# Kernel optimization log

Hardware: AMD Instinct MI355X
Metric: run time of the kernel (lower is better)

Reference implementation:

```python
import jax, jax.numpy as jnp
import numpy as np

H_DIM = 256
NUM_HEADS = 8
HEAD_DIM = H_DIM // NUM_HEADS
BN_EPS = 1e-5
SCALE = float(np.sqrt(HEAD_DIM))


def _lens():
    # 512 graphs, ragged vertex counts cycling 32/64/96/128 -> 40960 total rows
    return np.tile(np.array([32, 64, 96, 128], dtype=np.int64), 128)


def _pad(x, lens):
    # gather ragged rows of x [total, D] into padded [B, Lmax, D]; mask [B, Lmax]
    B = lens.shape[0]
    L = int(lens.max())
    off = np.zeros(B, np.int64)
    off[1:] = np.cumsum(lens)[:-1]
    pos = np.arange(L)
    idx = off[:, None] + np.minimum(pos[None, :], lens[:, None] - 1)
    mask = pos[None, :] < lens[:, None]
    return x[jnp.asarray(idx)], jnp.asarray(mask)


def _flat_idx(lens):
    # (graph_id, position) for every real row, to un-pad back to ragged layout
    b = np.repeat(np.arange(lens.shape[0]), lens)
    i = np.concatenate([np.arange(int(l)) for l in lens])
    return jnp.asarray(b), jnp.asarray(i)


def _forward(src_h, dst_h, src_lens, dst_lens,
             W1, b1, gamma1, beta1, W2, b2, gamma2, beta2):
    src_pad, src_mask = _pad(src_h, src_lens)   # [B, Ls, H]
    dst_pad, _ = _pad(dst_h, dst_lens)          # [B, Ld, H]
    B, Ls, _ = src_pad.shape
    Ld = dst_pad.shape[1]
    # NOTE: original torch code zips self.proj but never applies it, so
    # q = raw dst, k = v = raw src.  The .view(1, head_dim, heads, N) on the
    # channel-major tensor splits feature f as f = d*NUM_HEADS + h.
    q = dst_pad.reshape(B, Ld, HEAD_DIM, NUM_HEADS)
    k = src_pad.reshape(B, Ls, HEAD_DIM, NUM_HEADS)
    v = k
    scores = jnp.einsum('bndh,bmdh->bhnm', q, k) / SCALE
    scores = jnp.where(src_mask[:, None, None, :], scores, jnp.float32(-1e30))
    attn = jax.nn.softmax(scores, axis=-1)
    out = jnp.einsum('bhnm,bmdh->bndh', attn, v).reshape(B, Ld, H_DIM)
    bidx, iidx = _flat_idx(dst_lens)
    h_msg = out[bidx, iidx]                     # [total_dst, H] ragged again
    h = dst_h
    z = jnp.concatenate([h, h_msg], axis=-1)    # [N, 2H]
    y = z @ W1.T + b1
    y = gamma1 * (y - y.mean(0)) * jax.lax.rsqrt(y.var(0) + BN_EPS) + beta1
    y = jax.nn.relu(y)
    y = y @ W2.T + b2
    y = gamma2 * (y - y.mean(0)) * jax.lax.rsqrt(y.var(0) + BN_EPS) + beta2
    return h + y


def setup_inputs() -> dict:
    lens = _lens()
    N = int(lens.sum())
    ks = jax.random.split(jax.random.key(0), 4)
    return {
        'src_h': jax.random.normal(ks[0], (N, H_DIM), jnp.float32),
        'dst_h': jax.random.normal(ks[1], (N, H_DIM), jnp.float32),
        'src_num_verts': jnp.asarray(lens, jnp.int32),
        'dst_num_verts': jnp.asarray(lens, jnp.int32),
        'W1': jax.random.normal(ks[2], (H_DIM, 2 * H_DIM), jnp.float32) / np.float32(np.sqrt(2 * H_DIM)),
        'b1': jnp.zeros((H_DIM,), jnp.float32),
        'gamma1': jnp.ones((H_DIM,), jnp.float32),
        'beta1': jnp.zeros((H_DIM,), jnp.float32),
        'W2': jax.random.normal(ks[3], (H_DIM, H_DIM), jnp.float32) / np.float32(np.sqrt(H_DIM)),
        'b2': jnp.zeros((H_DIM,), jnp.float32),
        'gamma2': jnp.ones((H_DIM,), jnp.float32),
        'beta2': jnp.zeros((H_DIM,), jnp.float32),
    }


def reference(src_h, dst_h, src_num_verts, dst_num_verts,
              W1, b1, gamma1, beta1, W2, b2, gamma2, beta2):
    # segment lengths are static metadata (torch.split takes a Python list)
    src_lens = np.asarray(jax.device_get(src_num_verts), np.int64)
    dst_lens = np.asarray(jax.device_get(dst_num_verts), np.int64)
    return _forward(src_h, dst_h, src_lens, dst_lens,
                    W1, b1, gamma1, beta1, W2, b2, gamma2, beta2)
```

## Files before the change

kernel.cpp:

```cpp
#include <hip/hip_runtime.h>
#include <cstddef>

#define H 256
#define NHEADS 8
#define HD 32

typedef __attribute__((ext_vector_type(8))) short bf16x8;
typedef __attribute__((ext_vector_type(4))) float f32x4;

__device__ __forceinline__ float bf2f(unsigned short s) {
    unsigned u = ((unsigned)s) << 16; return __builtin_bit_cast(float, u);
}
__device__ __forceinline__ float bfe2f(short s) {
    unsigned u = ((unsigned)(unsigned short)s) << 16; return __builtin_bit_cast(float, u);
}
__device__ __forceinline__ unsigned short f2bf(float x) {
    unsigned u = __builtin_bit_cast(unsigned, x);
    u += 0x7fffu + ((u >> 16) & 1u);
    return (unsigned short)(u >> 16);
}
__device__ __forceinline__ void gl_lds16(const void* g, void* l) {
    __builtin_amdgcn_global_load_lds(
        (const __attribute__((address_space(1))) void*)g,
        (__attribute__((address_space(3))) void*)l, 16, 0, 0);
}

__global__ __launch_bounds__(512) void scan_zero_kernel(
    const int* __restrict__ slen, const int* __restrict__ dlen,
    int* __restrict__ soff, int* __restrict__ doff,
    float* __restrict__ stats, int B)
{
    __shared__ int ss[512], dd[512];
    const int t = threadIdx.x;
    const int sv = (t < B) ? slen[t] : 0;
    const int dv = (t < B) ? dlen[t] : 0;
    ss[t] = sv; dd[t] = dv;
    __syncthreads();
    for (int o = 1; o < 512; o <<= 1) {
        int a = (t >= o) ? ss[t - o] : 0;
        int b = (t >= o) ? dd[t - o] : 0;
        __syncthreads();
        ss[t] += a; dd[t] += b;
        __syncthreads();
    }
    if (t < B) { soff[t] = ss[t] - sv; doff[t] = dd[t] - dv; }
    stats[t] = 0.f;
    stats[t + 512] = 0.f;
}

__global__ __launch_bounds__(256) void prepass_kernel(
    const float* __restrict__ src, const float* __restrict__ dst,
    unsigned short* __restrict__ KT, unsigned short* __restrict__ VT2,
    unsigned short* __restrict__ QT, int N)
{
    __shared__ unsigned short pl[8 * 64 * 40];
    const int t = threadIdx.x;
    const int rb = blockIdx.x * 64;
    const int isrc = (blockIdx.y == 0);
    const float* __restrict__ in = isrc ? src : dst;
    unsigned short* __restrict__ T = isrc ? KT : QT;
    #pragma unroll
    for (int i = 0; i < 16; ++i) {
        const int idx = t + i * 256;
        const int row = idx >> 6, f4 = idx & 63;
        const float4 v = ((const float4*)in)[(size_t)(rb + row) * 64 + f4];
        const int f0 = f4 * 4, h0 = f0 & 7, d = f0 >> 3;
        pl[(h0 + 0) * 2560 + row * 40 + d] = f2bf(v.x);
        pl[(h0 + 1) * 2560 + row * 40 + d] = f2bf(v.y);
        pl[(h0 + 2) * 2560 + row * 40 + d] = f2bf(v.z);
        pl[(h0 + 3) * 2560 + row * 40 + d] = f2bf(v.w);
    }
    __syncthreads();
    #pragma unroll
    for (int i = 0; i < 8; ++i) {
        const int idx = t + i * 256;
        const int h = idx >> 8, rem = idx & 255, row = rem >> 2, c = rem & 3;
        const bf16x8 val = *(const bf16x8*)&pl[h * 2560 + row * 40 + c * 8];
        *(bf16x8*)&T[(size_t)(h * N + rb + row) * 32 + c * 8] = val;
    }
    if (isrc) {
        #pragma unroll
        for (int i = 0; i < 8; ++i) {
            const int idx = t + i * 256;
            const int h = idx >> 8, rem = idx & 255, d = rem >> 3, nc = rem & 7;
            unsigned short tmp[8];
            #pragma unroll
            for (int j = 0; j < 8; ++j) tmp[j] = pl[h * 2560 + (nc * 8 + j) * 40 + d];
            ushort4 lo, hi;
            lo.x = tmp[0]; lo.y = tmp[1]; lo.z = tmp[2]; lo.w = tmp[3];
            hi.x = tmp[4]; hi.y = tmp[5]; hi.z = tmp[6]; hi.w = tmp[7];
            *(ushort4*)&VT2[(size_t)(h * 32 + d) * N + rb + nc * 8] = lo;
            *(ushort4*)&VT2[(size_t)(h * 32 + d) * N + rb + nc * 8 + 4] = hi;
        }
    }
}

__global__ __launch_bounds__(256) void cvtW_kernel(
    const float* __restrict__ W1, const float* __restrict__ W2,
    unsigned short* __restrict__ W1p, unsigned short* __restrict__ W2bf)
{
    const int idx = blockIdx.x * 256 + threadIdx.x;
    if (idx < 131072) {
        const int kp = idx & 511, c = idx >> 9;
        const int half = kp >> 8, r = kp & 255, hh = r >> 5, d = r & 31;
        W1p[(size_t)c * 512 + kp] = f2bf(W1[(size_t)c * 512 + half * 256 + d * 8 + hh]);
    } else {
        const int i2 = idx - 131072;
        W2bf[i2] = f2bf(W2[i2]);
    }
}

template<int LS>
__device__ __forceinline__ void attn_body(
    const unsigned short* __restrict__ KT, const unsigned short* __restrict__ QT,
    const unsigned short* __restrict__ VT2, unsigned short* __restrict__ OT,
    unsigned short* __restrict__ Ps, int N, int so, int df, int Ld, int h, int lane)
{
    constexpr int MT = LS / 16, CH = LS / 32;
    const int lr = lane & 15, lq = lane >> 4;
    const float iscale = 0.17677669529663687f;

    bf16x8 kf[MT];
    #pragma unroll
    for (int mt = 0; mt < MT; ++mt)
        kf[mt] = *(const bf16x8*)&KT[(size_t)(h * N + so + mt * 16 + lr) * 32 + lq * 8];
    bf16x8 vf[CH][2];
    #pragma unroll
    for (int c = 0; c < CH; ++c)
        #pragma unroll
        for (int dt = 0; dt < 2; ++dt)
            vf[c][dt] = *(const bf16x8*)&VT2[(size_t)(h * 32 + dt * 16 + lr) * N + so + c * 32 + lq * 8];

    const int NT = Ld >> 4;
    for (int nt = 0; nt < NT; ++nt) {
        const bf16x8 qf = *(const bf16x8*)&QT[(size_t)(h * N + df + nt * 16 + lr) * 32 + lq * 8];
        f32x4 s[MT];
        #pragma unroll
        for (int mt = 0; mt < MT; ++mt) {
            f32x4 z = {0.f, 0.f, 0.f, 0.f};
            s[mt] = __builtin_amdgcn_mfma_f32_16x16x32_bf16(kf[mt], qf, z, 0, 0, 0);
        }
        float mx = -INFINITY;
        #pragma unroll
        for (int mt = 0; mt < MT; ++mt)
            mx = fmaxf(mx, fmaxf(fmaxf(s[mt][0], s[mt][1]), fmaxf(s[mt][2], s[mt][3])));
        mx = fmaxf(mx, __shfl_xor(mx, 16));
        mx = fmaxf(mx, __shfl_xor(mx, 32));
        const float mxi = mx * iscale;
        float sum = 0.f;
        #pragma unroll
        for (int mt = 0; mt < MT; ++mt) {
            #pragma unroll
            for (int r = 0; r < 4; ++r) {
                const float e = __expf(s[mt][r] * iscale - mxi);
                s[mt][r] = e; sum += e;
            }
        }
        sum += __shfl_xor(sum, 16);
        sum += __shfl_xor(sum, 32);
        const float rinv = 1.f / sum;
        #pragma unroll
        for (int mt = 0; mt < MT; ++mt) {
            uint2 p;
            p.x = ((unsigned)f2bf(s[mt][0])) | (((unsigned)f2bf(s[mt][1])) << 16);
            p.y = ((unsigned)f2bf(s[mt][2])) | (((unsigned)f2bf(s[mt][3])) << 16);
            *(uint2*)&Ps[lr * 136 + mt * 16 + lq * 4] = p;
        }
        __asm__ volatile("" ::: "memory");
        __builtin_amdgcn_wave_barrier();
        f32x4 o0 = {0.f, 0.f, 0.f, 0.f}, o1 = {0.f, 0.f, 0.f, 0.f};
        #pragma unroll
        for (int c = 0; c < CH; ++c) {
            const bf16x8 pa = *(const bf16x8*)&Ps[lr * 136 + c * 32 + lq * 8];
            o0 = __builtin_amdgcn_mfma_f32_16x16x32_bf16(pa, vf[c][0], o0, 0, 0, 0);
            o1 = __builtin_amdgcn_mfma_f32_16x16x32_bf16(pa, vf[c][1], o1, 0, 0, 0);
        }
        __asm__ volatile("" ::: "memory");
        __builtin_amdgcn_wave_barrier();
        #pragma unroll
        for (int r = 0; r < 4; ++r) {
            const float rv = __shfl(rinv, lq * 4 + r);
            const int row = df + nt * 16 + lq * 4 + r;
            OT[(size_t)(h * N + row) * 32 + lr]      = f2bf(o0[r] * rv);
            OT[(size_t)(h * N + row) * 32 + 16 + lr] = f2bf(o1[r] * rv);
        }
    }
}

__global__ __launch_bounds__(256) void attn_mfma(
    const unsigned short* __restrict__ KT, const unsigned short* __restrict__ QT,
    const unsigned short* __restrict__ VT2, unsigned short* __restrict__ OT,
    const int* __restrict__ soff, const int* __restrict__ doff,
    const int* __restrict__ slen, const int* __restrict__ dlen, int N)
{
    __shared__ unsigned short Ps[4][16 * 136];
    const int b = blockIdx.x >> 1, half = blockIdx.x & 1;
    const int w = threadIdx.x >> 6, lane = threadIdx.x & 63;
    const int h = half * 4 + w;
    const int Ls = slen[b], Ld = dlen[b], so = soff[b], df = doff[b];
    switch (Ls) {
        case 32:  attn_body<32> (KT, QT, VT2, OT, Ps[w], N, so, df, Ld, h, lane); break;
        case 64:  attn_body<64> (KT, QT, VT2, OT, Ps[w], N, so, df, Ld, h, lane); break;
        case 96:  attn_body<96> (KT, QT, VT2, OT, Ps[w], N, so, df, Ld, h, lane); break;
        default:  attn_body<128>(KT, QT, VT2, OT, Ps[w], N, so, df, Ld, h, lane); break;
    }
}

__global__ __launch_bounds__(256) void gemm1_mfma(
    const unsigned short* __restrict__ QT, const unsigned short* __restrict__ OT,
    const unsigned short* __restrict__ W, const float* __restrict__ bias,
    unsigned short* __restrict__ out, float* __restrict__ sum, float* __restrict__ sq,
    int N)
{
    __shared__ unsigned short Abuf[8 * 512];
    __shared__ unsigned short Bbuf[8 * 512];
    const int tid = threadIdx.x;
    const int w = tid >> 6, lane = tid & 63;
    const int rowBase = blockIdx.y * 128, colBase = blockIdx.x * 128;
    const int lr = lane & 15, lq = lane >> 4;
    const int wm = w >> 1, wn = w & 1;

    f32x4 acc[4][4];
    #pragma unroll
    for (int i = 0; i < 4; ++i)
        #pragma unroll
        for (int j = 0; j < 4; ++j) { f32x4 z = {0.f, 0.f, 0.f, 0.f}; acc[i][j] = z; }

    #pragma unroll
    for (int phase = 0; phase < 2; ++phase) {
        const unsigned short* __restrict__ Ap = phase ? OT : QT;
        const int wOff = phase * 256;
        for (int kb = 0; kb < 256; kb += 32) {
            const int hh = (kb >> 5) + (lq >> 2);
            const int dd = (lq & 3) * 8;
            #pragma unroll
            for (int s = 0; s < 2; ++s) {
                const int sub = 2 * w + s;
                const unsigned short* ga = Ap + (size_t)(hh * N + rowBase + sub * 16 + lr) * 32 + dd;
                gl_lds16(ga, &Abuf[sub * 512]);
                const unsigned short* gb = W + (size_t)(colBase + sub * 16 + lr) * 512 + wOff + kb + lq * 8;
                gl_lds16(gb, &Bbuf[sub * 512]);
            }
            __syncthreads();
            bf16x8 af[4], bf[4];
            #pragma unroll
            for (int i = 0; i < 4; ++i) af[i] = *(const bf16x8*)&Abuf[(wm * 4 + i) * 512 + lane * 8];
            #pragma unroll
            for (int j = 0; j < 4; ++j) bf[j] = *(const bf16x8*)&Bbuf[(wn * 4 + j) * 512 + lane * 8];
            #pragma unroll
            for (int i = 0; i < 4; ++i)
                #pragma unroll
                for (int j = 0; j < 4; ++j)
                    acc[i][j] = __builtin_amdgcn_mfma_f32_16x16x32_bf16(af[i], bf[j], acc[i][j], 0, 0, 0);
            __syncthreads();
        }
    }
    const int col0 = colBase + wn * 64;
    #pragma unroll
    for (int j = 0; j < 4; ++j) {
        const int col = col0 + j * 16 + lr;
        const float bv = bias[col];
        float cs = 0.f, cq = 0.f;
        #pragma unroll
        for (int i = 0; i < 4; ++i) {
            const int row0 = rowBase + wm * 64 + i * 16 + lq * 4;
            #pragma unroll
            for (int r = 0; r < 4; ++r) {
                const float v = acc[i][j][r] + bv;
                cs += v; cq += v * v;
                out[(size_t)(row0 + r) * 256 + col] = f2bf(v);
            }
        }
        cs += __shfl_xor(cs, 16); cs += __shfl_xor(cs, 32);
        cq += __shfl_xor(cq, 16); cq += __shfl_xor(cq, 32);
        if (lq == 0) { atomicAdd(&sum[col], cs); atomicAdd(&sq[col], cq); }
    }
}

__global__ __launch_bounds__(256) void gemm2_mfma(
    const unsigned short* __restrict__ A2,
    const unsigned short* __restrict__ W, const float* __restrict__ bias,
    unsigned short* __restrict__ out, float* __restrict__ sum, float* __restrict__ sq)
{
    __shared__ unsigned short Abuf[8 * 512];
    __shared__ unsigned short Bbuf[8 * 512];
    const int tid = threadIdx.x;
    const int w = tid >> 6, lane = tid & 63;
    const int rowBase = blockIdx.y * 128, colBase = blockIdx.x * 128;
    const int lr = lane & 15, lq = lane >> 4;
    const int wm = w >> 1, wn = w & 1;

    f32x4 acc[4][4];
    #pragma unroll
    for (int i = 0; i < 4; ++i)
        #pragma unroll
        for (int j = 0; j < 4; ++j) { f32x4 z = {0.f, 0.f, 0.f, 0.f}; acc[i][j] = z; }

    for (int kb = 0; kb < 256; kb += 32) {
        #pragma unroll
        for (int s = 0; s < 2; ++s) {
            const int sub = 2 * w + s;
            const unsigned short* ga = A2 + (size_t)(rowBase + sub * 16 + lr) * 256 + kb + lq * 8;
            gl_lds16(ga, &Abuf[sub * 512]);
            const unsigned short* gb = W + (size_t)(colBase + sub * 16 + lr) * 256 + kb + lq * 8;
            gl_lds16(gb, &Bbuf[sub * 512]);
        }
        __syncthreads();
        bf16x8 af[4], bf[4];
        #pragma unroll
        for (int i = 0; i < 4; ++i) af[i] = *(const bf16x8*)&Abuf[(wm * 4 + i) * 512 + lane * 8];
        #pragma unroll
        for (int j = 0; j < 4; ++j) bf[j] = *(const bf16x8*)&Bbuf[(wn * 4 + j) * 512 + lane * 8];
        #pragma unroll
        for (int i = 0; i < 4; ++i)
            #pragma unroll
            for (int j = 0; j < 4; ++j)
                acc[i][j] = __builtin_amdgcn_mfma_f32_16x16x32_bf16(af[i], bf[j], acc[i][j], 0, 0, 0);
        __syncthreads();
    }
    const int col0 = colBase + wn * 64;
    #pragma unroll
    for (int j = 0; j < 4; ++j) {
        const int col = col0 + j * 16 + lr;
        const float bv = bias[col];
        float cs = 0.f, cq = 0.f;
        #pragma unroll
        for (int i = 0; i < 4; ++i) {
            const int row0 = rowBase + wm * 64 + i * 16 + lq * 4;
            #pragma unroll
            for (int r = 0; r < 4; ++r) {
                const float v = acc[i][j][r] + bv;
                cs += v; cq += v * v;
                out[(size_t)(row0 + r) * 256 + col] = f2bf(v);
            }
        }
        cs += __shfl_xor(cs, 16); cs += __shfl_xor(cs, 32);
        cq += __shfl_xor(cq, 16); cq += __shfl_xor(cq, 32);
        if (lq == 0) { atomicAdd(&sum[col], cs); atomicAdd(&sq[col], cq); }
    }
}

__global__ __launch_bounds__(256) void bnrelu_kernel(
    const unsigned short* __restrict__ y1,
    const float* __restrict__ sum, const float* __restrict__ sq,
    const float* __restrict__ gamma, const float* __restrict__ beta,
    unsigned short* __restrict__ out, int n8, float invN)
{
    const int i = blockIdx.x * 256 + threadIdx.x;
    if (i >= n8) return;
    const int j0 = (i & 31) * 8;
    const bf16x8 yv = ((const bf16x8*)y1)[i];
    short res[8];
    #pragma unroll
    for (int j = 0; j < 8; ++j) {
        const float mean = sum[j0 + j] * invN;
        const float var  = sq[j0 + j] * invN - mean * mean;
        const float rstd = rsqrtf(var + 1e-5f);
        const float sc = gamma[j0 + j] * rstd;
        const float sh = beta[j0 + j] - mean * sc;
        res[j] = (short)f2bf(fmaxf(bfe2f(yv[j]) * sc + sh, 0.f));
    }
    bf16x8 o;
    #pragma unroll
    for (int j = 0; j < 8; ++j) o[j] = res[j];
    ((bf16x8*)out)[i] = o;
}

__global__ __launch_bounds__(256) void epilogue_kernel(
    const float* __restrict__ dst, const unsigned short* __restrict__ y2,
    const float* __restrict__ sum, const float* __restrict__ sq,
    const float* __restrict__ gamma, const float* __restrict__ beta,
    float* __restrict__ out, int n8, float invN)
{
    const int i = blockIdx.x * 256 + threadIdx.x;
    if (i >= n8) return;
    const int j0 = (i & 31) * 8;
    const bf16x8 yv = ((const bf16x8*)y2)[i];
    const float4 d0 = ((const float4*)dst)[2 * i];
    const float4 d1 = ((const float4*)dst)[2 * i + 1];
    float o[8];
    const float dv[8] = {d0.x, d0.y, d0.z, d0.w, d1.x, d1.y, d1.z, d1.w};
    #pragma unroll
    for (int j = 0; j < 8; ++j) {
        const float mean = sum[j0 + j] * invN;
        const float var  = sq[j0 + j] * invN - mean * mean;
        const float rstd = rsqrtf(var + 1e-5f);
        const float sc = gamma[j0 + j] * rstd;
        const float sh = beta[j0 + j] - mean * sc;
        o[j] = dv[j] + bfe2f(yv[j]) * sc + sh;
    }
    float4 o0, o1;
    o0.x = o[0]; o0.y = o[1]; o0.z = o[2]; o0.w = o[3];
    o1.x = o[4]; o1.y = o[5]; o1.z = o[6]; o1.w = o[7];
    ((float4*)out)[2 * i]     = o0;
    ((float4*)out)[2 * i + 1] = o1;
}

extern "C" void kernel_launch(void* const* d_in, const int* in_sizes, int n_in,
                              void* d_out, int out_size, void* d_ws, size_t ws_size,
                              hipStream_t stream)
{
    const float* src_h  = (const float*)d_in[0];
    const float* dst_h  = (const float*)d_in[1];
    const int*   slen   = (const int*)d_in[2];
    const int*   dlen   = (const int*)d_in[3];
    const float* W1     = (const float*)d_in[4];
    const float* b1     = (const float*)d_in[5];
    const float* gamma1 = (const float*)d_in[6];
    const float* beta1  = (const float*)d_in[7];
    const float* W2     = (const float*)d_in[8];
    const float* b2     = (const float*)d_in[9];
    const float* gamma2 = (const float*)d_in[10];
    const float* beta2  = (const float*)d_in[11];
    float* out = (float*)d_out;

    const int N = in_sizes[1] / H;
    const int B = in_sizes[2];

    char* base = (char*)d_ws;
    int*   soff   = (int*)(base + 0);
    int*   doff   = (int*)(base + 2048);
    float* stats  = (float*)(base + 4096);
    unsigned short* W1p  = (unsigned short*)(base + 16384);
    unsigned short* W2bf = (unsigned short*)(base + 16384 + 262144);
    const size_t S = (size_t)N * H * sizeof(unsigned short);
    char* big = base + (1 << 20);
    unsigned short* KT  = (unsigned short*)(big);
    unsigned short* VT2 = (unsigned short*)(big + S);
    unsigned short* QT  = (unsigned short*)(big + 2 * S);
    unsigned short* OT  = (unsigned short*)(big + 3 * S);
    unsigned short* y1bf = KT;
    unsigned short* a2   = VT2;
    unsigned short* y2bf = QT;

    const float invN = 1.0f / (float)N;

    scan_zero_kernel<<<1, 512, 0, stream>>>(slen, dlen, soff, doff, stats, B);

    prepass_kernel<<<dim3(N / 64, 2), 256, 0, stream>>>(src_h, dst_h, KT, VT2, QT, N);
    cvtW_kernel<<<768, 256, 0, stream>>>(W1, W2, W1p, W2bf);

    attn_mfma<<<B * 2, 256, 0, stream>>>(KT, QT, VT2, OT, soff, doff, slen, dlen, N);

    dim3 ggrid(H / 128, N / 128);
    gemm1_mfma<<<ggrid, 256, 0, stream>>>(QT, OT, W1p, b1, y1bf, stats + 0, stats + 256, N);

    const int n8 = N * H / 8;
    bnrelu_kernel<<<(n8 + 255) / 256, 256, 0, stream>>>(
        y1bf, stats + 0, stats + 256, gamma1, beta1, a2, n8, invN);

    gemm2_mfma<<<ggrid, 256, 0, stream>>>(a2, W2bf, b2, y2bf, stats + 512, stats + 768);

    epilogue_kernel<<<(n8 + 255) / 256, 256, 0, stream>>>(
        dst_h, y2bf, stats + 512, stats + 768, gamma2, beta2, out, n8, invN);
}
```

Measured before the change: 283.6 us.

## Fuse BN1+ReLU into GEMM2 and load MFMA operands directly from global

Drops the standalone BN/ReLU pass by applying the first batch-norm scale/shift and ReLU to Y1 as operands are loaded inside the second GEMM. Both GEMMs now load fragments straight from global memory into registers instead of staging through LDS with global_load_lds and barriers. Operand roles are swapped so outputs are written as 4-wide vectors, and column stats use a shuffle reduction across rows. This removes a full read/write pass over the hidden activations and a launch. In exchange there is no LDS reuse across waves, so global/L2 traffic per block rises, and GEMM2 does extra ALU work per loaded element.

Measured after the change: 409.1 us. 1.44x slower.

```diff
diff --git a/kernel.cpp b/kernel.cpp
--- a/kernel.cpp
+++ b/kernel.cpp
@@ -8,9 +8,6 @@
 typedef __attribute__((ext_vector_type(8))) short bf16x8;
 typedef __attribute__((ext_vector_type(4))) float f32x4;
 
-__device__ __forceinline__ float bf2f(unsigned short s) {
-    unsigned u = ((unsigned)s) << 16; return __builtin_bit_cast(float, u);
-}
 __device__ __forceinline__ float bfe2f(short s) {
     unsigned u = ((unsigned)(unsigned short)s) << 16; return __builtin_bit_cast(float, u);
 }
@@ -18,11 +15,6 @@
     unsigned u = __builtin_bit_cast(unsigned, x);
     u += 0x7fffu + ((u >> 16) & 1u);
     return (unsigned short)(u >> 16);
-}
-__device__ __forceinline__ void gl_lds16(const void* g, void* l) {
-    __builtin_amdgcn_global_load_lds(
-        (const __attribute__((address_space(1))) void*)g,
-        (__attribute__((address_space(3))) void*)l, 16, 0, 0);
 }
 
 __global__ __launch_bounds__(512) void scan_zero_kernel(
@@ -206,19 +198,18 @@
     }
 }
 
-__global__ __launch_bounds__(256) void gemm1_mfma(
+__global__ __launch_bounds__(256) void gemm1_direct(
     const unsigned short* __restrict__ QT, const unsigned short* __restrict__ OT,
     const unsigned short* __restrict__ W, const float* __restrict__ bias,
     unsigned short* __restrict__ out, float* __restrict__ sum, float* __restrict__ sq,
     int N)
 {
-    __shared__ unsigned short Abuf[8 * 512];
-    __shared__ unsigned short Bbuf[8 * 512];
     const int tid = threadIdx.x;
     const int w = tid >> 6, lane = tid & 63;
-    const int rowBase = blockIdx.y * 128, colBase = blockIdx.x * 128;
     const int lr = lane & 15, lq = lane >> 4;
     const int wm = w >> 1, wn = w & 1;
+    const int actBase = blockIdx.y * 128 + wm * 64;
+    const int colBase = blockIdx.x * 128 + wn * 64;
 
     f32x4 acc[4][4];
     #pragma unroll
@@ -226,69 +217,75 @@
         #pragma unroll
         for (int j = 0; j < 4; ++j) { f32x4 z = {0.f, 0.f, 0.f, 0.f}; acc[i][j] = z; }
 
-    #pragma unroll
-    for (int phase = 0; phase < 2; ++phase) {
-        const unsigned short* __restrict__ Ap = phase ? OT : QT;
-        const int wOff = phase * 256;
-        for (int kb = 0; kb < 256; kb += 32) {
-            const int hh = (kb >> 5) + (lq >> 2);
-            const int dd = (lq & 3) * 8;
-            #pragma unroll
-            for (int s = 0; s < 2; ++s) {
-                const int sub = 2 * w + s;
-                const unsigned short* ga = Ap + (size_t)(hh * N + rowBase + sub * 16 + lr) * 32 + dd;
-                gl_lds16(ga, &Abuf[sub * 512]);
-                const unsigned short* gb = W + (size_t)(colBase + sub * 16 + lr) * 512 + wOff + kb + lq * 8;
-                gl_lds16(gb, &Bbuf[sub * 512]);
-            }
-            __syncthreads();
-            bf16x8 af[4], bf[4];
-            #pragma unroll
-            for (int i = 0; i < 4; ++i) af[i] = *(const bf16x8*)&Abuf[(wm * 4 + i) * 512 + lane * 8];
-            #pragma unroll
-            for (int j = 0; j < 4; ++j) bf[j] = *(const bf16x8*)&Bbuf[(wn * 4 + j) * 512 + lane * 8];
-            #pragma unroll
-            for (int i = 0; i < 4; ++i)
-                #pragma unroll
-                for (int j = 0; j < 4; ++j)
-                    acc[i][j] = __builtin_amdgcn_mfma_f32_16x16x32_bf16(af[i], bf[j], acc[i][j], 0, 0, 0);
-            __syncthreads();
-        }
-    }
-    const int col0 = colBase + wn * 64;
-    #pragma unroll
-    for (int j = 0; j < 4; ++j) {
-        const int col = col0 + j * 16 + lr;
-        const float bv = bias[col];
-        float cs = 0.f, cq = 0.f;
-        #pragma unroll
-        for (int i = 0; i < 4; ++i) {
-            const int row0 = rowBase + wm * 64 + i * 16 + lq * 4;
-            #pragma unroll
-            for (int r = 0; r < 4; ++r) {
-                const float v = acc[i][j][r] + bv;
-                cs += v; cq += v * v;
-                out[(size_t)(row0 + r) * 256 + col] = f2bf(v);
-            }
-        }
-        cs += __shfl_xor(cs, 16); cs += __shfl_xor(cs, 32);
-        cq += __shfl_xor(cq, 16); cq += __shfl_xor(cq, 32);
-        if (lq == 0) { atomicAdd(&sum[col], cs); atomicAdd(&sq[col], cq); }
-    }
-}
-
-__global__ __launch_bounds__(256) void gemm2_mfma(
-    const unsigned short* __restrict__ A2,
+    for (int kk = 0; kk < 16; ++kk) {
+        const unsigned short* __restrict__ actp = (kk < 8) ? QT : OT;
+        const int hh = kk & 7;
+        bf16x8 aw[4], ba[4];
+        #pragma unroll
+        for (int i = 0; i < 4; ++i)
+            aw[i] = *(const bf16x8*)&W[(size_t)(colBase + i * 16 + lr) * 512 + kk * 32 + lq * 8];
+        #pragma unroll
+        for (int j = 0; j < 4; ++j)
+            ba[j] = *(const bf16x8*)&actp[(size_t)(hh * N + actBase + j * 16 + lr) * 32 + lq * 8];
+        #pragma unroll
+        for (int i = 0; i < 4; ++i)
+            #pragma unroll
+            for (int j = 0; j < 4; ++j)
+                acc[i][j] = __builtin_amdgcn_mfma_f32_16x16x32_bf16(aw[i], ba[j], acc[i][j], 0, 0, 0);
+    }
+
+    #pragma unroll
+    for (int i = 0; i < 4; ++i) {
+        const int c0 = colBase + i * 16 + lq * 4;
+        const float4 b4 = *(const float4*)&bias[c0];
+        float cs[4] = {0.f, 0.f, 0.f, 0.f}, cq[4] = {0.f, 0.f, 0.f, 0.f};
+        #pragma unroll
+        for (int j = 0; j < 4; ++j) {
+            const int row = actBase + j * 16 + lr;
+            float v[4];
+            v[0] = acc[i][j][0] + b4.x; v[1] = acc[i][j][1] + b4.y;
+            v[2] = acc[i][j][2] + b4.z; v[3] = acc[i][j][3] + b4.w;
+            ushort4 o;
+            o.x = f2bf(v[0]); o.y = f2bf(v[1]); o.z = f2bf(v[2]); o.w = f2bf(v[3]);
+            *(ushort4*)&out[(size_t)row * 256 + c0] = o;
+            #pragma unroll
+            for (int r = 0; r < 4; ++r) { cs[r] += v[r]; cq[r] += v[r] * v[r]; }
+        }
+        #pragma unroll
+        for (int r = 0; r < 4; ++r) {
+            float s = cs[r], q = cq[r];
+            s += __shfl_xor(s, 1); s += __shfl_xor(s, 2); s += __shfl_xor(s, 4); s += __shfl_xor(s, 8);
+            q += __shfl_xor(q, 1); q += __shfl_xor(q, 2); q += __shfl_xor(q, 4); q += __shfl_xor(q, 8);
+            if (lr == 0) { atomicAdd(&sum[c0 + r], s); atomicAdd(&sq[c0 + r], q); }
+        }
+    }
+}
+
+__global__ __launch_bounds__(256) void gemm2_direct(
+    const unsigned short* __restrict__ Y1,
     const unsigned short* __restrict__ W, const float* __restrict__ bias,
-    unsigned short* __restrict__ out, float* __restrict__ sum, float* __restrict__ sq)
-{
-    __shared__ unsigned short Abuf[8 * 512];
-    __shared__ unsigned short Bbuf[8 * 512];
+    const float* __restrict__ sum1, const float* __restrict__ sq1,
+    const float* __restrict__ gamma1, const float* __restrict__ beta1,
+    unsigned short* __restrict__ out, float* __restrict__ sum, float* __restrict__ sq,
+    float invN)
+{
+    __shared__ float sc1s[256], sh1s[256];
     const int tid = threadIdx.x;
+    {
+        const float mean = sum1[tid] * invN;
+        const float var  = sq1[tid] * invN - mean * mean;
+        const float rstd = rsqrtf(var + 1e-5f);
+        const float s = gamma1[tid] * rstd;
+        sc1s[tid] = s;
+        sh1s[tid] = beta1[tid] - mean * s;
+    }
+    __syncthreads();
+
     const int w = tid >> 6, lane = tid & 63;
-    const int rowBase = blockIdx.y * 128, colBase = blockIdx.x * 128;
     const int lr = lane & 15, lq = lane >> 4;
     const int wm = w >> 1, wn = w & 1;
+    const int actBase = blockIdx.y * 128 + wm * 64;
+    const int colBase = blockIdx.x * 128 + wn * 64;
 
     f32x4 acc[4][4];
     #pragma unroll
@@ -296,74 +293,59 @@
         #pragma unroll
         for (int j = 0; j < 4; ++j) { f32x4 z = {0.f, 0.f, 0.f, 0.f}; acc[i][j] = z; }
 
-    for (int kb = 0; kb < 256; kb += 32) {
-        #pragma unroll
-        for (int s = 0; s < 2; ++s) {
-            const int sub = 2 * w + s;
-            const unsigned short* ga = A2 + (size_t)(rowBase + sub * 16 + lr) * 256 + kb + lq * 8;
-            gl_lds16(ga, &Abuf[sub * 512]);
-            const unsigned short* gb = W + (size_t)(colBase + sub * 16 + lr) * 256 + kb + lq * 8;
-            gl_lds16(gb, &Bbuf[sub * 512]);
-        }
-        __syncthreads();
-        bf16x8 af[4], bf[4];
-        #pragma unroll
-        for (int i = 0; i < 4; ++i) af[i] = *(const bf16x8*)&Abuf[(wm * 4 + i) * 512 + lane * 8];
-        #pragma unroll
-        for (int j = 0; j < 4; ++j) bf[j] = *(const bf16x8*)&Bbuf[(wn * 4 + j) * 512 + lane * 8];
+    for (int kk = 0; kk < 8; ++kk) {
+        const int kc0 = kk * 32 + lq * 8;
+        const float4 sA = *(const float4*)&sc1s[kc0];
+        const float4 sB = *(const float4*)&sc1s[kc0 + 4];
+        const float4 hA = *(const float4*)&sh1s[kc0];
+        const float4 hB = *(const float4*)&sh1s[kc0 + 4];
+        const float sc[8] = {sA.x, sA.y, sA.z, sA.w, sB.x, sB.y, sB.z, sB.w};
+        const float sh[8] = {hA.x, hA.y, hA.z, hA.w, hB.x, hB.y, hB.z, hB.w};
+        bf16x8 aw[4], ba[4];
         #pragma unroll
         for (int i = 0; i < 4; ++i)
+            aw[i] = *(const bf16x8*)&W[(size_t)(colBase + i * 16 + lr) * 256 + kc0];
+        #pragma unroll
+        for (int j = 0; j < 4; ++j) {
+            const bf16x8 raw = *(const bf16x8*)&Y1[(size_t)(actBase + j * 16 + lr) * 256 + kc0];
+            bf16x8 bb;
+            #pragma unroll
+            for (int t = 0; t < 8; ++t)
+                bb[t] = (short)f2bf(fmaxf(bfe2f(raw[t]) * sc[t] + sh[t], 0.f));
+            ba[j] = bb;
+        }
+        #pragma unroll
+        for (int i = 0; i < 4; ++i)
             #pragma unroll
             for (int j = 0; j < 4; ++j)
-                acc[i][j] = __builtin_amdgcn_mfma_f32_16x16x32_bf16(af[i], bf[j], acc[i][j], 0, 0, 0);
-        __syncthreads();
-    }
-    const int col0 = colBase + wn * 64;
-    #pragma unroll
-    for (int j = 0; j < 4; ++j) {
-        const int col = col0 + j * 16 + lr;
-        const float bv = bias[col];
-        float cs = 0.f, cq = 0.f;
-        #pragma unroll
-        for (int i = 0; i < 4; ++i) {
-            const int row0 = rowBase + wm * 64 + i * 16 + lq * 4;
-            #pragma unroll
-            for (int r = 0; r < 4; ++r) {
-                const float v = acc[i][j][r] + bv;
-                cs += v; cq += v * v;
-                out[(size_t)(row0 + r) * 256 + col] = f2bf(v);
-            }
-        }
-        cs += __shfl_xor(cs, 16); cs += __shfl_xor(cs, 32);
-        cq += __shfl_xor(cq, 16); cq += __shfl_xor(cq, 32);
-        if (lq == 0) { atomicAdd(&sum[col], cs); atomicAdd(&sq[col], cq); }
-    }
-}
-
-__global__ __launch_bounds__(256) void bnrelu_kernel(
-    const unsigned short* __restrict__ y1,
-    const float* __restrict__ sum, const float* __restrict__ sq,
-    const float* __restrict__ gamma, const float* __restrict__ beta,
-    unsigned short* __restrict__ out, int n8, float invN)
-{
-    const int i = blockIdx.x * 256 + threadIdx.x;
-    if (i >= n8) return;
-    const int j0 = (i & 31) * 8;
-    const bf16x8 yv = ((const bf16x8*)y1)[i];
-    short res[8];
-    #pragma unroll
-    for (int j = 0; j < 8; ++j) {
-        const float mean = sum[j0 + j] * invN;
-        const float var  = sq[j0 + j] * invN - mean * mean;
-        const float rstd = rsqrtf(var + 1e-5f);
-        const float sc = gamma[j0 + j] * rstd;
-        const float sh = beta[j0 + j] - mean * sc;
-        res[j] = (short)f2bf(fmaxf(bfe2f(yv[j]) * sc + sh, 0.f));
-    }
-    bf16x8 o;
-    #pragma unroll
-    for (int j = 0; j < 8; ++j) o[j] = res[j];
-    ((bf16x8*)out)[i] = o;
+                acc[i][j] = __builtin_amdgcn_mfma_f32_16x16x32_bf16(aw[i], ba[j], acc[i][j], 0, 0, 0);
+    }
+
+    #pragma unroll
+    for (int i = 0; i < 4; ++i) {
+        const int c0 = colBase + i * 16 + lq * 4;
+        const float4 b4 = *(const float4*)&bias[c0];
+        float cs[4] = {0.f, 0.f, 0.f, 0.f}, cq[4] = {0.f, 0.f, 0.f, 0.f};
+        #pragma unroll
+        for (int j = 0; j < 4; ++j) {
+            const int row = actBase + j * 16 + lr;
+            float v[4];
+            v[0] = acc[i][j][0] + b4.x; v[1] = acc[i][j][1] + b4.y;
+            v[2] = acc[i][j][2] + b4.z; v[3] = acc[i][j][3] + b4.w;
+            ushort4 o;
+            o.x = f2bf(v[0]); o.y = f2bf(v[1]); o.z = f2bf(v[2]); o.w = f2bf(v[3]);
+            *(ushort4*)&out[(size_t)row * 256 + c0] = o;
+            #pragma unroll
+            for (int r = 0; r < 4; ++r) { cs[r] += v[r]; cq[r] += v[r] * v[r]; }
+        }
+        #pragma unroll
+        for (int r = 0; r < 4; ++r) {
+            float s = cs[r], q = cq[r];
+            s += __shfl_xor(s, 1); s += __shfl_xor(s, 2); s += __shfl_xor(s, 4); s += __shfl_xor(s, 8);
+            q += __shfl_xor(q, 1); q += __shfl_xor(q, 2); q += __shfl_xor(q, 4); q += __shfl_xor(q, 8);
+            if (lr == 0) { atomicAdd(&sum[c0 + r], s); atomicAdd(&sq[c0 + r], q); }
+        }
+    }
 }
 
 __global__ __launch_bounds__(256) void epilogue_kernel(
@@ -430,7 +412,6 @@
     unsigned short* QT  = (unsigned short*)(big + 2 * S);
     unsigned short* OT  = (unsigned short*)(big + 3 * S);
     unsigned short* y1bf = KT;
-    unsigned short* a2   = VT2;
     unsigned short* y2bf = QT;
 
     const float invN = 1.0f / (float)N;
@@ -443,14 +424,12 @@
     attn_mfma<<<B * 2, 256, 0, stream>>>(KT, QT, VT2, OT, soff, doff, slen, dlen, N);
 
     dim3 ggrid(H / 128, N / 128);
-    gemm1_mfma<<<ggrid, 256, 0, stream>>>(QT, OT, W1p, b1, y1bf, stats + 0, stats + 256, N);
+    gemm1_direct<<<ggrid, 256, 0, stream>>>(QT, OT, W1p, b1, y1bf, stats + 0, stats + 256, N);
+
+    gemm2_direct<<<ggrid, 256, 0, stream>>>(y1bf, W2bf, b2, stats + 0, stats + 256,
+                                            gamma1, beta1, y2bf, stats + 512, stats + 768, invN);
 
     const int n8 = N * H / 8;
-    bnrelu_kernel<<<(n8 + 255) / 256, 256, 0, stream>>>(
-        y1bf, stats + 0, stats + 256, gamma1, beta1, a2, n8, invN);
-
-    gemm2_mfma<<<ggrid, 256, 0, stream>>>(a2, W2bf, b2, y2bf, stats + 512, stats + 768);
-
     epilogue_kernel<<<(n8 + 255) / 256, 256, 0, stream>>>(
         dst_h, y2bf, stats + 512, stats + 768, gamma2, beta2, out, n8, invN);
 }
```
